# Performance work log

Measured on AMD Instinct MI355X. Metric: run time of the kernel, lower is better.

Reference implementation:

```python
import jax, jax.numpy as jnp
import numpy as np

N = 50000      # rows of A == cols of A (square constraint/variable graph)
NNZ = 1_600_000
D = 128        # x_size == y_size == out_size (forced by the module's wiring)


def spmm(rows, cols, vals, X, n_out):
    # out[r] = sum_{e: rows[e]==r} vals[e] * X[cols[e]]
    return jax.ops.segment_sum(vals[:, None] * X[cols], rows, num_segments=n_out)


def _linear(z, w, b):
    return z @ w.T + b


def setup_inputs() -> dict:
    key = jax.random.key(0)
    ks = jax.random.split(key, 20)
    f = lambda i, shape, s=1.0: jax.random.normal(ks[i], shape, dtype=jnp.float32) * s
    w_scale = 1.0 / np.sqrt(D)
    return {
        "x": f(0, (N, D)),
        "y": f(1, (N, D)),
        "c": f(2, (N, 1)),
        "b": f(3, (N, 1)),
        "A_vals": f(4, (NNZ,)),
        "A_rows": jax.random.randint(ks[5], (NNZ,), 0, N),
        "A_cols": jax.random.randint(ks[6], (NNZ,), 0, N),
        "Ukx_w": f(7, (D, D), w_scale), "Ukx_b": f(8, (D,), w_scale),
        "Uky_w": f(9, (D, D), w_scale), "Uky_b": f(10, (D,), w_scale),
        "tau": f(11, (1,)),
        "Vky_w": f(12, (D, D), w_scale), "Vky_b": f(13, (D,), w_scale),
        "Wkx_w": f(14, (D, D), w_scale), "Wkx_b": f(15, (D,), w_scale),
        "Vkx_w": f(16, (D, D), w_scale), "Vkx_b": f(17, (D,), w_scale),
        "sigma": f(18, (1,)),
    }


def reference(x, y, c, b, A_vals, A_rows, A_cols,
              Ukx_w, Ukx_b, Uky_w, Uky_b, tau,
              Vky_w, Vky_b, Wkx_w, Wkx_b, Vkx_w, Vkx_b, sigma):
    # --- pdhg_layer_x: x <- relu(Ukx(x) - tau * (c @ ones(1,D) - AT @ Uky(y))) ---
    # c @ ones(1, D) is just broadcasting c:[N,1] to [N,D].
    uy = _linear(y, Uky_w, Uky_b)                      # [N, D]
    at_uy = spmm(A_cols, A_rows, A_vals, uy, N)        # AT spmm: swap row/col indices
    x_new = jax.nn.relu(_linear(x, Ukx_w, Ukx_b) - tau * (c - at_uy))

    # --- pdhg_layer_y: y <- relu(Vky(y) - sigma * (b@ones - 2*A@Wkx(x') + A@Vkx(x'))) ---
    wx = _linear(x_new, Wkx_w, Wkx_b)                  # [N, D]
    vx = _linear(x_new, Vkx_w, Vkx_b)                  # [N, D]
    a_wx = spmm(A_rows, A_cols, A_vals, wx, N)
    a_vx = spmm(A_rows, A_cols, A_vals, vx, N)
    y_new = jax.nn.relu(_linear(y, Vky_w, Vky_b) - sigma * (b - 2.0 * a_wx + a_vx))
    return (x_new, y_new)
```

## Files before the change

### kernel.cpp

```cpp
#include <hip/hip_runtime.h>

#define D 128
#define RB 256
#define NBKMAX 256
#define CH 256
#define LDSREC 6400

typedef __attribute__((ext_vector_type(4))) float f32x4;
typedef __attribute__((ext_vector_type(8))) short bf16x8;

__device__ __forceinline__ unsigned short bf16r(float f) {
    unsigned b = __float_as_uint(f);
    return (unsigned short)((b + 0x7FFFu + ((b >> 16) & 1u)) >> 16);
}

__global__ __launch_bounds__(256) void setup_weights(
    const float* __restrict__ Uky, const float* __restrict__ Ukx,
    const float* __restrict__ Vky, const float* __restrict__ Vkx,
    const float* __restrict__ Wkx, const float* __restrict__ Vkx_b,
    const float* __restrict__ Wkx_b,
    float* __restrict__ UkyT, float* __restrict__ UkxT,
    float* __restrict__ VkyT, float* __restrict__ WcT,
    unsigned short* __restrict__ UkyB, unsigned short* __restrict__ UkxB,
    unsigned short* __restrict__ VkyB, unsigned short* __restrict__ WcB,
    float* __restrict__ bc)
{
    const int m = blockIdx.x;
    if (m < 4) {
        const float* src = (m == 0) ? Uky : (m == 1) ? Ukx : (m == 2) ? Vky : nullptr;
        float* dst = (m == 0) ? UkyT : (m == 1) ? UkxT : (m == 2) ? VkyT : WcT;
        for (int i = threadIdx.x; i < D * D; i += 256) {
            int k = i >> 7, d = i & 127;
            float v;
            if (m == 3) v = Vkx[d * D + k] - 2.0f * Wkx[d * D + k];
            else        v = src[d * D + k];
            dst[i] = v;
        }
        if (m == 3 && threadIdx.x < D)
            bc[threadIdx.x] = Vkx_b[threadIdx.x] - 2.0f * Wkx_b[threadIdx.x];
    } else {
        const int mm = m - 4;
        const float* src = (mm == 0) ? Uky : (mm == 1) ? Ukx : (mm == 2) ? Vky : nullptr;
        unsigned short* dst = (mm == 0) ? UkyB : (mm == 1) ? UkxB : (mm == 2) ? VkyB : WcB;
        for (int i = threadIdx.x; i < D * D; i += 256) {
            float v;
            if (mm == 3) v = Vkx[i] - 2.0f * Wkx[i];
            else         v = src[i];
            dst[i] = bf16r(v);
        }
    }
}

template <int EPI, int OB16>
__global__ __launch_bounds__(256) void gemm_mfma(
    const float* __restrict__ X, const unsigned short* __restrict__ Wb,
    const float* __restrict__ bias, const float* __restrict__ colvec,
    const float* __restrict__ spout, const float* __restrict__ scal,
    float* __restrict__ out, int N)
{
    __shared__ __align__(16) unsigned short Xs[64 * 128];
    const int t = threadIdx.x;
    const int block_row = blockIdx.x * 64;

#pragma unroll
    for (int i = 0; i < 8; ++i) {
        int f = t + i * 256;
        int r = f >> 5;
        int k4 = (f & 31) << 2;
        float4 g = make_float4(0.f, 0.f, 0.f, 0.f);
        int row = block_row + r;
        if (row < N) g = *reinterpret_cast<const float4*>(&X[(size_t)row * D + k4]);
        ushort4 h;
        h.x = bf16r(g.x); h.y = bf16r(g.y); h.z = bf16r(g.z); h.w = bf16r(g.w);
        unsigned byte = (unsigned)(k4 * 2) ^ ((unsigned)(r & 7) << 4);
        *reinterpret_cast<ushort4*>((char*)Xs + r * 256 + byte) = h;
    }
    __syncthreads();

    const int w  = t >> 6;
    const int l  = t & 63;
    const int lr = l & 15;
    const int lq = l >> 4;

    f32x4 acc[8];
#pragma unroll
    for (int nt = 0; nt < 8; ++nt) acc[nt] = (f32x4)(0.f);

    const int arow = w * 16 + lr;

#pragma unroll
    for (int kc = 0; kc < 4; ++kc) {
        unsigned abyte = ((unsigned)(kc * 64 + lq * 16)) ^ ((unsigned)(arow & 7) << 4);
        bf16x8 a = *reinterpret_cast<const bf16x8*>((const char*)Xs + arow * 256 + abyte);
#pragma unroll
        for (int nt = 0; nt < 8; ++nt) {
            bf16x8 b = *reinterpret_cast<const bf16x8*>(
                &Wb[(size_t)(nt * 16 + lr) * D + kc * 32 + lq * 8]);
            acc[nt] = __builtin_amdgcn_mfma_f32_16x16x32_bf16(a, b, acc[nt], 0, 0, 0);
        }
    }

    const float sc = (EPI == 0) ? 0.f : scal[0];
    float bs[8];
#pragma unroll
    for (int nt = 0; nt < 8; ++nt) bs[nt] = bias[nt * 16 + lr];

#pragma unroll
    for (int r = 0; r < 4; ++r) {
        const int row = block_row + w * 16 + lq * 4 + r;
        if (row >= N) continue;
        const float cv = (EPI == 0) ? 0.f : colvec[row];
#pragma unroll
        for (int nt = 0; nt < 8; ++nt) {
            const int col = nt * 16 + lr;
            float res = acc[nt][r] + bs[nt];
            if (EPI == 1) {
                float sp = spout[(size_t)row * D + col];
                res = fmaxf(res - sc * (cv - sp), 0.f);
            } else if (EPI == 2) {
                float sp = spout[(size_t)row * D + col];
                res = fmaxf(res - sc * (cv + sp), 0.f);
            }
            if (OB16) ((unsigned short*)out)[(size_t)row * D + col] = bf16r(res);
            else      out[(size_t)row * D + col] = res;
        }
    }
}

template <int EPI>
__global__ __launch_bounds__(256) void gemm_v2(
    const float* __restrict__ X, const float* __restrict__ WT,
    const float* __restrict__ bias, const float* __restrict__ colvec,
    const float* __restrict__ spout, const float* __restrict__ scal,
    float* __restrict__ out, int N)
{
    __shared__ float Xsf[64][D + 4];
    __shared__ float Wt[64][D + 4];
    const int t = threadIdx.x;
    const int block_row = blockIdx.x * 64;

#pragma unroll
    for (int i = 0; i < 8; ++i) {
        int f = t + i * 256;
        int r = f >> 5;
        int k4 = (f & 31) << 2;
        float4 g = make_float4(0.f, 0.f, 0.f, 0.f);
        int row = block_row + r;
        if (row < N) g = *reinterpret_cast<const float4*>(&X[(size_t)row * D + k4]);
        *reinterpret_cast<float4*>(&Xsf[r][k4]) = g;
    }

    const int cg = t & 15;
    const int rp = t >> 4;
    const int r0 = rp * 4;
    const int c0 = cg * 4, c1 = 64 + cg * 4;
    float acc[4][8] = {{0.f}};

    for (int kb = 0; kb < D; kb += 64) {
        __syncthreads();
#pragma unroll
        for (int i = 0; i < 8; ++i) {
            int f = t + i * 256;
            int kk = f >> 5;
            int d4 = (f & 31) << 2;
            float4 g = *reinterpret_cast<const float4*>(&WT[(size_t)(kb + kk) * D + d4]);
            *reinterpret_cast<float4*>(&Wt[kk][d4]) = g;
        }
        __syncthreads();
#pragma unroll 2
        for (int k4 = 0; k4 < 64; k4 += 4) {
            float4 xr[4];
#pragma unroll
            for (int j = 0; j < 4; ++j)
                xr[j] = *reinterpret_cast<const float4*>(&Xsf[r0 + j][kb + k4]);
#pragma unroll
            for (int q = 0; q < 4; ++q) {
                const float4 w0 = *reinterpret_cast<const float4*>(&Wt[k4 + q][c0]);
                const float4 w1 = *reinterpret_cast<const float4*>(&Wt[k4 + q][c1]);
#pragma unroll
                for (int j = 0; j < 4; ++j) {
                    const float xv = (q == 0) ? xr[j].x : (q == 1) ? xr[j].y
                                   : (q == 2) ? xr[j].z : xr[j].w;
                    acc[j][0] += xv * w0.x; acc[j][1] += xv * w0.y;
                    acc[j][2] += xv * w0.z; acc[j][3] += xv * w0.w;
                    acc[j][4] += xv * w1.x; acc[j][5] += xv * w1.y;
                    acc[j][6] += xv * w1.z; acc[j][7] += xv * w1.w;
                }
            }
        }
    }

    const float sc = (EPI == 0) ? 0.f : scal[0];
    const float4 bias0 = *reinterpret_cast<const float4*>(&bias[c0]);
    const float4 bias1 = *reinterpret_cast<const float4*>(&bias[c1]);

#pragma unroll
    for (int j = 0; j < 4; ++j) {
        const int row = block_row + r0 + j;
        if (row >= N) continue;
        const float cv = (EPI == 0) ? 0.f : colvec[row];
#pragma unroll
        for (int h = 0; h < 2; ++h) {
            const int col = (h == 0) ? c0 : c1;
            const float4 bsv = (h == 0) ? bias0 : bias1;
            float4 res;
            res.x = acc[j][h * 4 + 0] + bsv.x;
            res.y = acc[j][h * 4 + 1] + bsv.y;
            res.z = acc[j][h * 4 + 2] + bsv.z;
            res.w = acc[j][h * 4 + 3] + bsv.w;
            if (EPI == 1) {
                float4 sp = *reinterpret_cast<const float4*>(&spout[(size_t)row * D + col]);
                res.x = fmaxf(res.x - sc * (cv - sp.x), 0.f);
                res.y = fmaxf(res.y - sc * (cv - sp.y), 0.f);
                res.z = fmaxf(res.z - sc * (cv - sp.z), 0.f);
                res.w = fmaxf(res.w - sc * (cv - sp.w), 0.f);
            } else if (EPI == 2) {
                float4 sp = *reinterpret_cast<const float4*>(&spout[(size_t)row * D + col]);
                res.x = fmaxf(res.x - sc * (cv + sp.x), 0.f);
                res.y = fmaxf(res.y - sc * (cv + sp.y), 0.f);
                res.z = fmaxf(res.z - sc * (cv + sp.z), 0.f);
                res.w = fmaxf(res.w - sc * (cv + sp.w), 0.f);
            }
            *reinterpret_cast<float4*>(&out[(size_t)row * D + col]) = res;
        }
    }
}

__global__ __launch_bounds__(256) void hist_chunks(
    const int* __restrict__ rows, const int* __restrict__ cols,
    int* __restrict__ hR, int* __restrict__ hC, int nnz, int nbk, int ce)
{
    __shared__ int lh[NBKMAX];
    const int chunk = blockIdx.x;
    const bool isC = blockIdx.y;
    const int* idx = isC ? cols : rows;
    int* hout = (isC ? hC : hR) + (size_t)chunk * nbk;
    for (int i = threadIdx.x; i < nbk; i += 256) lh[i] = 0;
    __syncthreads();
    const int e0 = chunk * ce, e1 = min(nnz, e0 + ce);
    for (int e = e0 + threadIdx.x; e < e1; e += 256)
        atomicAdd(&lh[idx[e] >> 8], 1);
    __syncthreads();
    for (int i = threadIdx.x; i < nbk; i += 256) hout[i] = lh[i];
}

__global__ __launch_bounds__(256) void bucket_tot(
    const int* __restrict__ hR, const int* __restrict__ hC,
    int* __restrict__ cntR, int* __restrict__ cntC, int nbk)
{
    const int b = blockIdx.x;
    const bool isC = blockIdx.y;
    const int* h = (isC ? hC : hR);
    __shared__ int s[256];
    int v = h[(size_t)threadIdx.x * nbk + b];
    s[threadIdx.x] = v;
    __syncthreads();
#pragma unroll
    for (int d = 128; d > 0; d >>= 1) {
        if (threadIdx.x < d) s[threadIdx.x] += s[threadIdx.x + d];
        __syncthreads();
    }
    if (threadIdx.x == 0) (isC ? cntC : cntR)[b] = s[0];
}

__global__ __launch_bounds__(256) void scan_buckets(
    const int* __restrict__ cntR, const int* __restrict__ cntC,
    int* __restrict__ goffR, int* __restrict__ goffC, int nbk)
{
    const int* cnt = blockIdx.x ? cntC : cntR;
    int* goff = blockIdx.x ? goffC : goffR;
    __shared__ int s[256];
    const int t = threadIdx.x;
    int v = (t < nbk) ? cnt[t] : 0;
    s[t] = v;
    __syncthreads();
#pragma unroll
    for (int d = 1; d < 256; d <<= 1) {
        int tv = (t >= d) ? s[t - d] : 0;
        __syncthreads();
        s[t] += tv;
        __syncthreads();
    }
    if (t < nbk) goff[t] = s[t] - v;
}

__global__ __launch_bounds__(256) void runstarts(
    const int* __restrict__ hR, const int* __restrict__ hC,
    int* __restrict__ rsR, int* __restrict__ rsC,
    const int* __restrict__ goffR, const int* __restrict__ goffC, int nbk)
{
    const int b = blockIdx.x;
    const bool isC = blockIdx.y;
    const int* h = (isC ? hC : hR);
    int* rs = (isC ? rsC : rsR);
    const int g0 = (isC ? goffC : goffR)[b];
    __shared__ int s[256];
    const int t = threadIdx.x;
    int v = h[(size_t)t * nbk + b];
    s[t] = v;
    __syncthreads();
#pragma unroll
    for (int d = 1; d < 256; d <<= 1) {
        int tv = (t >= d) ? s[t - d] : 0;
        __syncthreads();
        s[t] += tv;
        __syncthreads();
    }
    rs[(size_t)t * nbk + b] = g0 + s[t] - v;
}

__global__ __launch_bounds__(256) void scatter_sorted(
    const int* __restrict__ rows, const int* __restrict__ cols,
    const float* __restrict__ vals,
    const int* __restrict__ hR, const int* __restrict__ rsR, int2* __restrict__ recR,
    const int* __restrict__ hC, const int* __restrict__ rsC, int2* __restrict__ recC,
    int nnz, int nbk, int ce)
{
    __shared__ int2 recL[LDSREC];
    __shared__ unsigned char bktL[LDSREC];
    __shared__ int lpos[NBKMAX], lcur[NBKMAX], lrs[NBKMAX], ssc[256];
    const int t = threadIdx.x;
    const int chunk = blockIdx.x;
    const bool isC = blockIdx.y;
    const int* h  = isC ? hC : hR;
    const int* rs = isC ? rsC : rsR;
    int2* recG    = isC ? recC : recR;
    const int e0 = chunk * ce, e1 = min(nnz, e0 + ce);
    const int Lc = e1 - e0;

    int v = (t < nbk) ? h[(size_t)chunk * nbk + t] : 0;
    if (t < nbk) lrs[t] = rs[(size_t)chunk * nbk + t];
    ssc[t] = v;
    __syncthreads();
#pragma unroll
    for (int d = 1; d < 256; d <<= 1) {
        int tv = (t >= d) ? ssc[t - d] : 0;
        __syncthreads();
        ssc[t] += tv;
        __syncthreads();
    }
    if (t < nbk) { lpos[t] = ssc[t] - v; lcur[t] = 0; }
    __syncthreads();

    for (int e = e0 + t; e < e1; e += 256) {
        int r = rows[e], c = cols[e];
        int dst  = isC ? c : r;
        int gcol = isC ? r : c;
        int b = dst >> 8;
        int q = atomicAdd(&lcur[b], 1);
        int slot = lpos[b] + q;
        recL[slot] = make_int2(((dst & 255) << 16) | gcol, __float_as_int(vals[e]));
        bktL[slot] = (unsigned char)b;
    }
    __syncthreads();

    for (int j = t; j < Lc; j += 256) {
        int b = bktL[j];
        recG[lrs[b] + (j - lpos[b])] = recL[j];
    }
}

__global__ __launch_bounds__(256) void sort_buckets(
    const int2* __restrict__ recR, const int2* __restrict__ recC,
    const int* __restrict__ goffR, const int* __restrict__ cntR,
    const int* __restrict__ goffC, const int* __restrict__ cntC,
    unsigned* __restrict__ pairsR, unsigned* __restrict__ pairsC,
    int* __restrict__ offR, int* __restrict__ lenR,
    int* __restrict__ offC, int* __restrict__ lenC, int N)
{
    const bool isC = blockIdx.y;
    const int b = blockIdx.x;
    const int2* rec = isC ? recC : recR;
    unsigned* pairs = isC ? pairsC : pairsR;
    int* off = isC ? offC : offR;
    int* len = isC ? lenC : lenR;
    const int s = (isC ? goffC : goffR)[b];
    const int L = (isC ? cntC : cntR)[b];
    const int t = threadIdx.x;

    __shared__ int lcnt[RB], lpos[RB], lcur[RB], sscan[256];
    lcnt[t] = 0;
    __syncthreads();
    for (int i = t; i < L; i += 256)
        atomicAdd(&lcnt[rec[s + i].x >> 16], 1);
    __syncthreads();
    {
        int v = lcnt[t];
        sscan[t] = v;
        __syncthreads();
#pragma unroll
        for (int d = 1; d < 256; d <<= 1) {
            int tv = (t >= d) ? sscan[t - d] : 0;
            __syncthreads();
            sscan[t] += tv;
            __syncthreads();
        }
        lpos[t] = sscan[t] - v;
    }
    {
        int row = b * RB + t;
        if (row < N) { off[row] = s + lpos[t]; len[row] = lcnt[t]; }
        lcur[t] = 0;
    }
    __syncthreads();
    for (int i = t; i < L; i += 256) {
        int2 pr = rec[s + i];
        int r = pr.x >> 16;
        int p = lpos[r] + atomicAdd(&lcur[r], 1);
        unsigned vb = (unsigned)pr.y;
        unsigned v16 = (vb + 0x7FFFu + ((vb >> 16) & 1u)) >> 16;
        pairs[s + p] = (v16 << 16) | (unsigned)(pr.x & 0xFFFF);
    }
}

__global__ __launch_bounds__(256) void spmm_pairs_v3(
    const unsigned* __restrict__ pairs, const int* __restrict__ off,
    const int* __restrict__ len, const unsigned short* __restrict__ Xb,
    float* __restrict__ out, int N)
{
    const int row = (blockIdx.x * 256 + threadIdx.x) >> 6;
    if (row >= N) return;
    const int lane = threadIdx.x & 63;
    const int half = lane >> 5;
    const int cq = (lane & 31) << 2;
    const int s = off[row];
    const int L = len[row];

    float4 a0 = make_float4(0.f, 0.f, 0.f, 0.f);
    float4 a1 = make_float4(0.f, 0.f, 0.f, 0.f);
    float4 a2 = make_float4(0.f, 0.f, 0.f, 0.f);
    float4 a3 = make_float4(0.f, 0.f, 0.f, 0.f);

#define BF(u) __uint_as_float((unsigned)(u) << 16)
    int i = 0;
    for (; i + 7 < L; i += 8) {
        unsigned p0 = pairs[s + i + 0 + half];
        unsigned p1 = pairs[s + i + 2 + half];
        unsigned p2 = pairs[s + i + 4 + half];
        unsigned p3 = pairs[s + i + 6 + half];
        ushort4 x0 = *reinterpret_cast<const ushort4*>(&Xb[(size_t)(p0 & 0xFFFFu) * D + cq]);
        ushort4 x1 = *reinterpret_cast<const ushort4*>(&Xb[(size_t)(p1 & 0xFFFFu) * D + cq]);
        ushort4 x2 = *reinterpret_cast<const ushort4*>(&Xb[(size_t)(p2 & 0xFFFFu) * D + cq]);
        ushort4 x3 = *reinterpret_cast<const ushort4*>(&Xb[(size_t)(p3 & 0xFFFFu) * D + cq]);
        float v0 = __uint_as_float(p0 & 0xFFFF0000u);
        float v1 = __uint_as_float(p1 & 0xFFFF0000u);
        float v2 = __uint_as_float(p2 & 0xFFFF0000u);
        float v3 = __uint_as_float(p3 & 0xFFFF0000u);
        a0.x += v0 * BF(x0.x); a0.y += v0 * BF(x0.y); a0.z += v0 * BF(x0.z); a0.w += v0 * BF(x0.w);
        a1.x += v1 * BF(x1.x); a1.y += v1 * BF(x1.y); a1.z += v1 * BF(x1.z); a1.w += v1 * BF(x1.w);
        a2.x += v2 * BF(x2.x); a2.y += v2 * BF(x2.y); a2.z += v2 * BF(x2.z); a2.w += v2 * BF(x2.w);
        a3.x += v3 * BF(x3.x); a3.y += v3 * BF(x3.y); a3.z += v3 * BF(x3.z); a3.w += v3 * BF(x3.w);
    }
    for (; i < L; i += 2) {
        int e = i + half;
        unsigned p = (e < L) ? pairs[s + e] : 0u;
        ushort4 xv = *reinterpret_cast<const ushort4*>(&Xb[(size_t)(p & 0xFFFFu) * D + cq]);
        float v = __uint_as_float(p & 0xFFFF0000u);
        a0.x += v * BF(xv.x); a0.y += v * BF(xv.y); a0.z += v * BF(xv.z); a0.w += v * BF(xv.w);
    }
#undef BF

    float4 A;
    A.x = (a0.x + a1.x) + (a2.x + a3.x);
    A.y = (a0.y + a1.y) + (a2.y + a3.y);
    A.z = (a0.z + a1.z) + (a2.z + a3.z);
    A.w = (a0.w + a1.w) + (a2.w + a3.w);
    A.x += __shfl_xor(A.x, 32);
    A.y += __shfl_xor(A.y, 32);
    A.z += __shfl_xor(A.z, 32);
    A.w += __shfl_xor(A.w, 32);
    if (half == 0)
        *reinterpret_cast<float4*>(&out[(size_t)row * D + cq]) = A;
}

__global__ __launch_bounds__(256) void spmm_atomic(
    const float* __restrict__ vals, const int* __restrict__ orow,
    const int* __restrict__ gcol, const float* __restrict__ Xm,
    float* __restrict__ outm, int nnz)
{
    const int gwave = (blockIdx.x * 256 + threadIdx.x) >> 6;
    const int lane = threadIdx.x & 63;
    const int e0 = gwave * 4;
#pragma unroll
    for (int i = 0; i < 4; ++i) {
        int e = e0 + i;
        if (e >= nnz) break;
        float v = vals[e];
        int r = orow[e];
        int c = gcol[e];
        float2 xv = *reinterpret_cast<const float2*>(&Xm[(size_t)c * D + lane * 2]);
        unsafeAtomicAdd(&outm[(size_t)r * D + lane * 2 + 0], v * xv.x);
        unsafeAtomicAdd(&outm[(size_t)r * D + lane * 2 + 1], v * xv.y);
    }
}

extern "C" void kernel_launch(void* const* d_in, const int* in_sizes, int n_in,
                              void* d_out, int out_size, void* d_ws, size_t ws_size,
                              hipStream_t stream) {
    const float* x      = (const float*)d_in[0];
    const float* y      = (const float*)d_in[1];
    const float* c      = (const float*)d_in[2];
    const float* b      = (const float*)d_in[3];
    const float* A_vals = (const float*)d_in[4];
    const int*   A_rows = (const int*)d_in[5];
    const int*   A_cols = (const int*)d_in[6];
    const float* Ukx_w  = (const float*)d_in[7];
    const float* Ukx_b  = (const float*)d_in[8];
    const float* Uky_w  = (const float*)d_in[9];
    const float* Uky_b  = (const float*)d_in[10];
    const float* tau    = (const float*)d_in[11];
    const float* Vky_w  = (const float*)d_in[12];
    const float* Vky_b  = (const float*)d_in[13];
    const float* Wkx_w  = (const float*)d_in[14];
    const float* Wkx_b  = (const float*)d_in[15];
    const float* Vkx_w  = (const float*)d_in[16];
    const float* Vkx_b  = (const float*)d_in[17];
    const float* sigma  = (const float*)d_in[18];

    const int N   = in_sizes[0] / D;
    const int nnz = in_sizes[4];
    const int nbk = (N + RB - 1) / RB;

    float* out_x = (float*)d_out;
    float* out_y = out_x + (size_t)N * D;

    const int gemm_grid = (N + 63) / 64;
    const int ggrid = (N + 3) / 4;
    const int ce = (nnz + CH - 1) / CH;

    const size_t pool = (size_t)nnz;
    char* base = (char*)d_ws;
    float* tmp = (float*)base;
    int2* recR = (int2*)base;
    int2* recC = recR + pool;
    size_t region0 = (size_t)N * D * 4;
    if (2 * pool * 8 > region0) region0 = 2 * pool * 8;
    char* pers = base + region0;
    float* UkyT = (float*)pers;
    float* UkxT = UkyT + D * D;
    float* VkyT = UkxT + D * D;
    float* WcT  = VkyT + D * D;
    unsigned short* UkyB = (unsigned short*)(WcT + D * D);
    unsigned short* UkxB = UkyB + D * D;
    unsigned short* VkyB = UkxB + D * D;
    unsigned short* WcB  = VkyB + D * D;
    float* bc = (float*)(WcB + D * D);
    unsigned* pairsR = (unsigned*)(bc + D);
    unsigned* pairsC = pairsR + pool;
    int* cntR  = (int*)(pairsC + pool);
    int* cntC  = cntR + nbk;
    int* goffR = cntC + nbk;
    int* goffC = goffR + nbk;
    int* offR  = goffC + nbk;
    int* lenR  = offR + N;
    int* offC  = lenR + N;
    int* lenC  = offC + N;
    int* hR  = (int*)pairsR;
    int* hC  = hR + (size_t)CH * nbk;
    int* rsR = hC + (size_t)CH * nbk;
    int* rsC = rsR + (size_t)CH * nbk;

    unsigned short* uyb = (unsigned short*)out_y;
    unsigned short* zxb = (unsigned short*)tmp;

    size_t need = region0 + (4 * (size_t)D * D + D) * 4 + 4 * (size_t)D * D * 2
                + 2 * pool * 4 + (4 * (size_t)nbk + 4 * (size_t)N) * 4;
    bool alias_fits = (size_t)4 * CH * nbk * 4 <= pool * 4;

    setup_weights<<<8, 256, 0, stream>>>(Uky_w, Ukx_w, Vky_w, Vkx_w, Wkx_w,
                                         Vkx_b, Wkx_b, UkyT, UkxT, VkyT, WcT,
                                         UkyB, UkxB, VkyB, WcB, bc);

    if (N < 65536 && nbk <= NBKMAX && ws_size >= need && alias_fits && ce <= LDSREC) {
        {
            dim3 g1(CH, 2);
            hist_chunks<<<g1, 256, 0, stream>>>(A_rows, A_cols, hR, hC, nnz, nbk, ce);
            dim3 g2(nbk, 2);
            bucket_tot<<<g2, 256, 0, stream>>>(hR, hC, cntR, cntC, nbk);
            scan_buckets<<<2, 256, 0, stream>>>(cntR, cntC, goffR, goffC, nbk);
            runstarts<<<g2, 256, 0, stream>>>(hR, hC, rsR, rsC, goffR, goffC, nbk);
            scatter_sorted<<<g1, 256, 0, stream>>>(A_rows, A_cols, A_vals,
                                                   hR, rsR, recR, hC, rsC, recC,
                                                   nnz, nbk, ce);
            sort_buckets<<<g2, 256, 0, stream>>>(recR, recC, goffR, cntR, goffC, cntC,
                                                 pairsR, pairsC, offR, lenR, offC, lenC, N);
        }

        gemm_mfma<0, 1><<<gemm_grid, 256, 0, stream>>>(y, UkyB, Uky_b, nullptr, nullptr, nullptr,
                                                       (float*)uyb, N);
        spmm_pairs_v3<<<ggrid, 256, 0, stream>>>(pairsC, offC, lenC, uyb, out_x, N);
        gemm_mfma<1, 0><<<gemm_grid, 256, 0, stream>>>(x, UkxB, Ukx_b, c, out_x, tau, out_x, N);
        gemm_mfma<0, 1><<<gemm_grid, 256, 0, stream>>>(out_x, WcB, bc, nullptr, nullptr, nullptr,
                                                       (float*)zxb, N);
        spmm_pairs_v3<<<ggrid, 256, 0, stream>>>(pairsR, offR, lenR, zxb, out_y, N);
        gemm_mfma<2, 0><<<gemm_grid, 256, 0, stream>>>(y, VkyB, Vky_b, b, out_y, sigma, out_y, N);
    } else {
        const int spmm_grid = (nnz + 15) / 16;
        gemm_v2<0><<<gemm_grid, 256, 0, stream>>>(y, UkyT, Uky_b, nullptr, nullptr, nullptr, tmp, N);
        hipMemsetAsync(out_x, 0, (size_t)N * D * sizeof(float), stream);
        spmm_atomic<<<spmm_grid, 256, 0, stream>>>(A_vals, A_cols, A_rows, tmp, out_x, nnz);
        gemm_v2<1><<<gemm_grid, 256, 0, stream>>>(x, UkxT, Ukx_b, c, out_x, tau, out_x, N);
        gemm_v2<0><<<gemm_grid, 256, 0, stream>>>(out_x, WcT, bc, nullptr, nullptr, nullptr, tmp, N);
        hipMemsetAsync(out_y, 0, (size_t)N * D * sizeof(float), stream);
        spmm_atomic<<<spmm_grid, 256, 0, stream>>>(A_vals, A_rows, A_cols, tmp, out_y, nnz);
        gemm_v2<2><<<gemm_grid, 256, 0, stream>>>(y, VkyT, Vky_b, b, out_y, sigma, out_y, N);
    }
}
```

Measured before the change: 283.3 us.

## Fuse x-update GEMM with combined W/V projection and deepen SpMM unroll

Adds a kernel that computes the relu x-update, writes it out, keeps the result as bf16 in shared memory, and immediately multiplies it by the combined Wkx/Vkx weights. This removes one launch and the global read of the freshly written x. Separately, the SpMM gather loop now issues 16 edges per iteration, putting more independent loads in flight at some cost in register pressure.

After: 288.0 us. Within noise of the previous version (+1.6%).

```diff
diff --git a/kernel.cpp b/kernel.cpp
--- a/kernel.cpp
+++ b/kernel.cpp
@@ -123,6 +123,108 @@
             }
             if (OB16) ((unsigned short*)out)[(size_t)row * D + col] = bf16r(res);
             else      out[(size_t)row * D + col] = res;
+        }
+    }
+}
+
+__global__ __launch_bounds__(256) void gemm_mfma_xz(
+    const float* __restrict__ X, const unsigned short* __restrict__ Wb,
+    const float* __restrict__ bias, const float* __restrict__ colvec,
+    const float* __restrict__ spout, const float* __restrict__ scal,
+    float* __restrict__ out,
+    const unsigned short* __restrict__ Wb2, const float* __restrict__ bias2,
+    unsigned short* __restrict__ out2, int N)
+{
+    __shared__ __align__(16) unsigned short Xs[64 * 128];
+    const int t = threadIdx.x;
+    const int block_row = blockIdx.x * 64;
+
+#pragma unroll
+    for (int i = 0; i < 8; ++i) {
+        int f = t + i * 256;
+        int r = f >> 5;
+        int k4 = (f & 31) << 2;
+        float4 g = make_float4(0.f, 0.f, 0.f, 0.f);
+        int row = block_row + r;
+        if (row < N) g = *reinterpret_cast<const float4*>(&X[(size_t)row * D + k4]);
+        ushort4 h;
+        h.x = bf16r(g.x); h.y = bf16r(g.y); h.z = bf16r(g.z); h.w = bf16r(g.w);
+        unsigned byte = (unsigned)(k4 * 2) ^ ((unsigned)(r & 7) << 4);
+        *reinterpret_cast<ushort4*>((char*)Xs + r * 256 + byte) = h;
+    }
+    __syncthreads();
+
+    const int w  = t >> 6;
+    const int l  = t & 63;
+    const int lr = l & 15;
+    const int lq = l >> 4;
+    const int arow = w * 16 + lr;
+
+    f32x4 acc[8];
+#pragma unroll
+    for (int nt = 0; nt < 8; ++nt) acc[nt] = (f32x4)(0.f);
+
+#pragma unroll
+    for (int kc = 0; kc < 4; ++kc) {
+        unsigned abyte = ((unsigned)(kc * 64 + lq * 16)) ^ ((unsigned)(arow & 7) << 4);
+        bf16x8 a = *reinterpret_cast<const bf16x8*>((const char*)Xs + arow * 256 + abyte);
+#pragma unroll
+        for (int nt = 0; nt < 8; ++nt) {
+            bf16x8 b = *reinterpret_cast<const bf16x8*>(
+                &Wb[(size_t)(nt * 16 + lr) * D + kc * 32 + lq * 8]);
+            acc[nt] = __builtin_amdgcn_mfma_f32_16x16x32_bf16(a, b, acc[nt], 0, 0, 0);
+        }
+    }
+    __syncthreads();
+
+    const float sc = scal[0];
+    float bs[8];
+#pragma unroll
+    for (int nt = 0; nt < 8; ++nt) bs[nt] = bias[nt * 16 + lr];
+
+#pragma unroll
+    for (int r = 0; r < 4; ++r) {
+        const int lrow = w * 16 + lq * 4 + r;
+        const int row = block_row + lrow;
+        const float cv = (row < N) ? colvec[row] : 0.f;
+#pragma unroll
+        for (int nt = 0; nt < 8; ++nt) {
+            const int col = nt * 16 + lr;
+            float res = 0.f;
+            if (row < N) {
+                float sp = spout[(size_t)row * D + col];
+                res = fmaxf(acc[nt][r] + bs[nt] - sc * (cv - sp), 0.f);
+                out[(size_t)row * D + col] = res;
+            }
+            unsigned byte = (unsigned)(col * 2) ^ ((unsigned)(lrow & 7) << 4);
+            *reinterpret_cast<unsigned short*>((char*)Xs + lrow * 256 + byte) = bf16r(res);
+        }
+    }
+    __syncthreads();
+
+#pragma unroll
+    for (int nt = 0; nt < 8; ++nt) acc[nt] = (f32x4)(0.f);
+#pragma unroll
+    for (int kc = 0; kc < 4; ++kc) {
+        unsigned abyte = ((unsigned)(kc * 64 + lq * 16)) ^ ((unsigned)(arow & 7) << 4);
+        bf16x8 a = *reinterpret_cast<const bf16x8*>((const char*)Xs + arow * 256 + abyte);
+#pragma unroll
+        for (int nt = 0; nt < 8; ++nt) {
+            bf16x8 b = *reinterpret_cast<const bf16x8*>(
+                &Wb2[(size_t)(nt * 16 + lr) * D + kc * 32 + lq * 8]);
+            acc[nt] = __builtin_amdgcn_mfma_f32_16x16x32_bf16(a, b, acc[nt], 0, 0, 0);
+        }
+    }
+#pragma unroll
+    for (int nt = 0; nt < 8; ++nt) bs[nt] = bias2[nt * 16 + lr];
+#pragma unroll
+    for (int r = 0; r < 4; ++r) {
+        const int row = block_row + w * 16 + lq * 4 + r;
+        if (row >= N) continue;
+#pragma unroll
+        for (int nt = 0; nt < 8; ++nt) {
+            const int col = nt * 16 + lr;
+            out2[(size_t)row * D + col] = bf16r(acc[nt][r] + bs[nt]);
         }
     }
 }
@@ -413,7 +515,7 @@
     }
 }
 
-__global__ __launch_bounds__(256) void spmm_pairs_v3(
+__global__ __launch_bounds__(256) void spmm_pairs_v4(
     const unsigned* __restrict__ pairs, const int* __restrict__ off,
     const int* __restrict__ len, const unsigned short* __restrict__ Xb,
     float* __restrict__ out, int N)
@@ -433,6 +535,40 @@
 
 #define BF(u) __uint_as_float((unsigned)(u) << 16)
     int i = 0;
+    for (; i + 15 < L; i += 16) {
+        unsigned p0 = pairs[s + i + 0 + half];
+        unsigned p1 = pairs[s + i + 2 + half];
+        unsigned p2 = pairs[s + i + 4 + half];
+        unsigned p3 = pairs[s + i + 6 + half];
+        unsigned p4 = pairs[s + i + 8 + half];
+        unsigned p5 = pairs[s + i + 10 + half];
+        unsigned p6 = pairs[s + i + 12 + half];
+        unsigned p7 = pairs[s + i + 14 + half];
+        ushort4 x0 = *reinterpret_cast<const ushort4*>(&Xb[(size_t)(p0 & 0xFFFFu) * D + cq]);
+        ushort4 x1 = *reinterpret_cast<const ushort4*>(&Xb[(size_t)(p1 & 0xFFFFu) * D + cq]);
+        ushort4 x2 = *reinterpret_cast<const ushort4*>(&Xb[(size_t)(p2 & 0xFFFFu) * D + cq]);
+        ushort4 x3 = *reinterpret_cast<const ushort4*>(&Xb[(size_t)(p3 & 0xFFFFu) * D + cq]);
+        ushort4 x4 = *reinterpret_cast<const ushort4*>(&Xb[(size_t)(p4 & 0xFFFFu) * D + cq]);
+        ushort4 x5 = *reinterpret_cast<const ushort4*>(&Xb[(size_t)(p5 & 0xFFFFu) * D + cq]);
+        ushort4 x6 = *reinterpret_cast<const ushort4*>(&Xb[(size_t)(p6 & 0xFFFFu) * D + cq]);
+        ushort4 x7 = *reinterpret_cast<const ushort4*>(&Xb[(size_t)(p7 & 0xFFFFu) * D + cq]);
+        float v0 = __uint_as_float(p0 & 0xFFFF0000u);
+        float v1 = __uint_as_float(p1 & 0xFFFF0000u);
+        float v2 = __uint_as_float(p2 & 0xFFFF0000u);
+        float v3 = __uint_as_float(p3 & 0xFFFF0000u);
+        float v4 = __uint_as_float(p4 & 0xFFFF0000u);
+        float v5 = __uint_as_float(p5 & 0xFFFF0000u);
+        float v6 = __uint_as_float(p6 & 0xFFFF0000u);
+        float v7 = __uint_as_float(p7 & 0xFFFF0000u);
+        a0.x += v0 * BF(x0.x); a0.y += v0 * BF(x0.y); a0.z += v0 * BF(x0.z); a0.w += v0 * BF(x0.w);
+        a1.x += v1 * BF(x1.x); a1.y += v1 * BF(x1.y); a1.z += v1 * BF(x1.z); a1.w += v1 * BF(x1.w);
+        a2.x += v2 * BF(x2.x); a2.y += v2 * BF(x2.y); a2.z += v2 * BF(x2.z); a2.w += v2 * BF(x2.w);
+        a3.x += v3 * BF(x3.x); a3.y += v3 * BF(x3.y); a3.z += v3 * BF(x3.z); a3.w += v3 * BF(x3.w);
+        a0.x += v4 * BF(x4.x); a0.y += v4 * BF(x4.y); a0.z += v4 * BF(x4.z); a0.w += v4 * BF(x4.w);
+        a1.x += v5 * BF(x5.x); a1.y += v5 * BF(x5.y); a1.z += v5 * BF(x5.z); a1.w += v5 * BF(x5.w);
+        a2.x += v6 * BF(x6.x); a2.y += v6 * BF(x6.y); a2.z += v6 * BF(x6.z); a2.w += v6 * BF(x6.w);
+        a3.x += v7 * BF(x7.x); a3.y += v7 * BF(x7.y); a3.z += v7 * BF(x7.z); a3.w += v7 * BF(x7.w);
+    }
     for (; i + 7 < L; i += 8) {
         unsigned p0 = pairs[s + i + 0 + half];
         unsigned p1 = pairs[s + i + 2 + half];
@@ -588,11 +724,10 @@
 
         gemm_mfma<0, 1><<<gemm_grid, 256, 0, stream>>>(y, UkyB, Uky_b, nullptr, nullptr, nullptr,
                                                        (float*)uyb, N);
-        spmm_pairs_v3<<<ggrid, 256, 0, stream>>>(pairsC, offC, lenC, uyb, out_x, N);
-        gemm_mfma<1, 0><<<gemm_grid, 256, 0, stream>>>(x, UkxB, Ukx_b, c, out_x, tau, out_x, N);
-        gemm_mfma<0, 1><<<gemm_grid, 256, 0, stream>>>(out_x, WcB, bc, nullptr, nullptr, nullptr,
-                                                       (float*)zxb, N);
-        spmm_pairs_v3<<<ggrid, 256, 0, stream>>>(pairsR, offR, lenR, zxb, out_y, N);
+        spmm_pairs_v4<<<ggrid, 256, 0, stream>>>(pairsC, offC, lenC, uyb, out_x, N);
+        gemm_mfma_xz<<<gemm_grid, 256, 0, stream>>>(x, UkxB, Ukx_b, c, out_x, tau, out_x,
+                                                    WcB, bc, zxb, N);
+        spmm_pairs_v4<<<ggrid, 256, 0, stream>>>(pairsR, offR, lenR, zxb, out_y, N);
         gemm_mfma<2, 0><<<gemm_grid, 256, 0, stream>>>(y, VkyB, Vky_b, b, out_y, sigma, out_y, N);
     } else {
         const int spmm_grid = (nnz + 15) / 16;
```
